# Kernel optimization log

Hardware: AMD Instinct MI355X
Metric: run time of the kernel (lower is better)

## Reference

```python
import jax, jax.numpy as jnp
import numpy as np

N = 50000   # nodes
E = 300000  # edges per etype
D = 256     # in_channels
STEPS = 3   # number_steps
EPS = 1e-5  # LayerNorm eps


def setup_inputs() -> dict:
    key = jax.random.key(0)
    ks = jax.random.split(key, 32)
    inp = {"x": jax.random.normal(ks[0], (N, D), jnp.float32)}
    for e in range(4):
        inp[f"src{e}"] = jax.random.randint(ks[1 + 2 * e], (E,), 0, N)
        inp[f"dst{e}"] = jax.random.randint(ks[2 + 2 * e], (E,), 0, N)
        inp[f"W{e}"] = jax.random.normal(ks[9 + e], (D, D), jnp.float32) / np.sqrt(D).astype(np.float32)
        inp[f"b{e}"] = jnp.zeros((D,), jnp.float32)
    inp["W_ih"] = jax.random.normal(ks[20], (3 * D, D), jnp.float32) / np.sqrt(D).astype(np.float32)
    inp["W_hh"] = jax.random.normal(ks[21], (3 * D, D), jnp.float32) / np.sqrt(D).astype(np.float32)
    inp["b_ih"] = jnp.zeros((3 * D,), jnp.float32)
    inp["b_hh"] = jnp.zeros((3 * D,), jnp.float32)
    inp["gamma"] = jnp.ones((D,), jnp.float32)
    inp["beta"] = jnp.zeros((D,), jnp.float32)
    return inp


def reference(x, src0, dst0, src1, dst1, src2, dst2, src3, dst3,
              W0, b0, W1, b1, W2, b2, W3, b3,
              W_ih, W_hh, b_ih, b_hh, gamma, beta):
    srcs = (src0, src1, src2, src3)
    dsts = (dst0, dst1, dst2, dst3)
    lins = ((W0, b0), (W1, b1), (W2, b2), (W3, b3))
    n_nodes = x.shape[0]

    def step(h):
        # per-etype: linear projection, gather on src, scatter-mean on dst; cross-etype 'sum'
        agg = jnp.zeros_like(h)
        for (W, b), s, d in zip(lins, srcs, dsts):
            proj = h @ W.T + b                                  # [N, D]
            msum = jax.ops.segment_sum(proj[s], d, num_segments=n_nodes)  # [N, D]
            deg = jax.ops.segment_sum(jnp.ones((s.shape[0], 1), h.dtype), d, num_segments=n_nodes)
            agg = agg + msum / jnp.maximum(deg, 1.0)            # mean; 0 for isolated nodes
        # torch GRUCell: input = agg, hidden = h
        gi = agg @ W_ih.T + b_ih                                # [N, 3D]
        gh = h @ W_hh.T + b_hh                                  # [N, 3D]
        i_r, i_z, i_n = jnp.split(gi, 3, axis=-1)
        h_r, h_z, h_n = jnp.split(gh, 3, axis=-1)
        r = jax.nn.sigmoid(i_r + h_r)
        z = jax.nn.sigmoid(i_z + h_z)
        n = jnp.tanh(i_n + r * h_n)
        h = (1.0 - z) * n + z * h
        # LayerNorm (use_norm=True); dropout is identity in eval mode
        mu = h.mean(-1, keepdims=True)
        var = h.var(-1, keepdims=True)
        return (h - mu) * jax.lax.rsqrt(var + EPS) * gamma + beta

    for _ in range(STEPS):
        x = step(x)
    return x
```

## Files before the change

### kernel.cpp

```cpp
#include <hip/hip_runtime.h>
#include <hip/hip_bf16.h>
#include <cstddef>

#define N_NODES 50000
#define E_EDGES 300000
#define D 256
#define SCHUNKS 196

typedef unsigned short u16;
typedef __attribute__((ext_vector_type(8))) short bf16x8;
typedef __attribute__((ext_vector_type(4))) float f32x4;

__device__ __forceinline__ float b2f(u16 u) {
    return __uint_as_float(((unsigned)u) << 16);
}
__device__ __forceinline__ u16 f2b(float f) {
    __hip_bfloat16 h = __float2bfloat16(f);
    return *reinterpret_cast<u16*>(&h);
}
__device__ __forceinline__ void async16(const u16* g, u16* l) {
    __builtin_amdgcn_global_load_lds(
        (const __attribute__((address_space(1))) void*)g,
        (__attribute__((address_space(3))) void*)l, 16, 0, 0);
}

__global__ __launch_bounds__(256) void prep_kernel(
    const float* __restrict__ W0, const float* __restrict__ W1,
    const float* __restrict__ W2, const float* __restrict__ W3,
    const float* __restrict__ b0, const float* __restrict__ b1,
    const float* __restrict__ b2, const float* __restrict__ b3,
    const float* __restrict__ W_ih, const float* __restrict__ W_hh,
    const float* __restrict__ b_ih, const float* __restrict__ b_hh,
    u16* __restrict__ Bfull_b, u16* __restrict__ Bcat_b,
    float* __restrict__ bfull, float* __restrict__ be4)
{
    int t = blockIdx.x * 256 + threadIdx.x;
    {
        int j = t >> 9, k = t & 511;
        float v;
        if (k < 256) v = (j < 768) ? W_ih[j * 256 + k] : W_hh[(j - 256) * 256 + k];
        else         v = (j < 512) ? W_hh[j * 256 + (k - 256)] : 0.f;
        Bfull_b[t] = f2b(v);
    }
    if (t < 262144) {
        int j = t >> 10, k = t & 1023;
        int e = k >> 8, kk = k & 255;
        const float* W = (e == 0) ? W0 : (e == 1) ? W1 : (e == 2) ? W2 : W3;
        Bcat_b[t] = f2b(W[j * 256 + kk]);
    }
    if (t < 1024) {
        bfull[t] = (t < 512) ? b_ih[t] + b_hh[t]
                 : (t < 768) ? b_ih[t] : b_hh[t - 256];
        int e = t >> 8, k = t & 255;
        const float* b = (e == 0) ? b0 : (e == 1) ? b1 : (e == 2) ? b2 : b3;
        be4[t] = b[k];
    }
}

__global__ __launch_bounds__(256) void xcvt_kernel(
    const float* __restrict__ x, u16* __restrict__ hb)
{
    int t = blockIdx.x * 256 + threadIdx.x;
    float4 v = *reinterpret_cast<const float4*>(x + (size_t)t * 4);
    ushort4 o;
    o.x = f2b(v.x); o.y = f2b(v.y); o.z = f2b(v.z); o.w = f2b(v.w);
    *reinterpret_cast<ushort4*>(hb + (size_t)t * 4) = o;
}

__global__ __launch_bounds__(256) void cnt_kernel(
    const int* __restrict__ d0, const int* __restrict__ d1,
    const int* __restrict__ d2, const int* __restrict__ d3,
    int* __restrict__ rowptr, u16* __restrict__ rank)
{
    int i = blockIdx.x * 256 + threadIdx.x;
    if (i >= 4 * E_EDGES) return;
    int e = i / E_EDGES;
    int k = i - e * E_EDGES;
    const int* dp = (e == 0) ? d0 : (e == 1) ? d1 : (e == 2) ? d2 : d3;
    rank[i] = (u16)atomicAdd(&rowptr[e * (N_NODES + 1) + dp[k] + 1], 1);
}

__global__ __launch_bounds__(256) void scan1_kernel(
    int* __restrict__ rowptr, int* __restrict__ bsum)
{
    int e = blockIdx.y;
    int blk = blockIdx.x;
    int t = threadIdx.x;
    int idx = blk * 256 + t;
    int* rp = rowptr + e * (N_NODES + 1);
    int v = (idx <= N_NODES) ? rp[idx] : 0;
    __shared__ int s[256];
    s[t] = v;
    __syncthreads();
    for (int o = 1; o < 256; o <<= 1) {
        int u = (t >= o) ? s[t - o] : 0;
        __syncthreads();
        s[t] += u;
        __syncthreads();
    }
    if (idx <= N_NODES) rp[idx] = s[t];
    if (t == 255) bsum[e * SCHUNKS + blk] = s[255];
}

__global__ __launch_bounds__(256) void scan2_kernel(int* __restrict__ bsum)
{
    int e = blockIdx.x;
    int t = threadIdx.x;
    int v = (t < SCHUNKS) ? bsum[e * SCHUNKS + t] : 0;
    __shared__ int s[256];
    s[t] = v;
    __syncthreads();
    for (int o = 1; o < 256; o <<= 1) {
        int u = (t >= o) ? s[t - o] : 0;
        __syncthreads();
        s[t] += u;
        __syncthreads();
    }
    if (t < SCHUNKS) bsum[e * SCHUNKS + t] = s[t];
}

__global__ __launch_bounds__(256) void scan3_kernel(
    int* __restrict__ rowptr, const int* __restrict__ bsum)
{
    int e = blockIdx.y;
    int blk = blockIdx.x;
    if (blk == 0) return;
    int idx = blk * 256 + threadIdx.x;
    if (idx > N_NODES) return;
    rowptr[e * (N_NODES + 1) + idx] += bsum[e * SCHUNKS + blk - 1];
}

__global__ __launch_bounds__(256) void fill_csr_kernel(
    const int* __restrict__ s0, const int* __restrict__ d0,
    const int* __restrict__ s1, const int* __restrict__ d1,
    const int* __restrict__ s2, const int* __restrict__ d2,
    const int* __restrict__ s3, const int* __restrict__ d3,
    const int* __restrict__ rowptr, const u16* __restrict__ rank,
    u16* __restrict__ colb)
{
    int i = blockIdx.x * 256 + threadIdx.x;
    if (i >= 4 * E_EDGES) return;
    int e = i / E_EDGES;
    int k = i - e * E_EDGES;
    const int* sp = (e == 0) ? s0 : (e == 1) ? s1 : (e == 2) ? s2 : s3;
    const int* dp = (e == 0) ? d0 : (e == 1) ? d1 : (e == 2) ? d2 : d3;
    int dst = dp[k];
    int slot = rowptr[e * (N_NODES + 1) + dst] + (int)rank[i];
    colb[(size_t)e * E_EDGES + slot] = (u16)sp[k];
}

__global__ __launch_bounds__(256) void degmask_kernel(
    const int* __restrict__ rowptr, unsigned char* __restrict__ degmask)
{
    int n = blockIdx.x * 256 + threadIdx.x;
    if (n >= N_NODES) return;
    int m = 0;
#pragma unroll
    for (int e = 0; e < 4; ++e) {
        const int* rp = rowptr + e * (N_NODES + 1);
        if (rp[n + 1] > rp[n]) m |= (1 << e);
    }
    degmask[n] = (unsigned char)m;
}

__global__ __launch_bounds__(256) void gather_kernel(
    const u16* __restrict__ hb, const int* __restrict__ rowptr,
    const u16* __restrict__ colb, u16* __restrict__ out,
    int pairArg, int stride)
{
    int p = (pairArg < 0) ? (int)blockIdx.y : pairArg;
    int n = blockIdx.x * 2 + (threadIdx.x >> 7);
    int el = (threadIdx.x >> 6) & 1;
    int lane = threadIdx.x & 63;
    int e = p * 2 + el;
    const int* rp = rowptr + e * (N_NODES + 1);
    int beg = rp[n], end = rp[n + 1];
    const u16* cb = colb + (size_t)e * E_EDGES;

    float4 a0 = make_float4(0.f, 0.f, 0.f, 0.f);
    float4 a1 = a0, a2 = a0, a3 = a0;
    int j = beg;
    for (; j + 4 <= end; j += 4) {
        int s0 = cb[j], s1 = cb[j + 1], s2 = cb[j + 2], s3 = cb[j + 3];
        ushort4 u0 = *reinterpret_cast<const ushort4*>(hb + (size_t)s0 * D + lane * 4);
        ushort4 u1 = *reinterpret_cast<const ushort4*>(hb + (size_t)s1 * D + lane * 4);
        ushort4 u2 = *reinterpret_cast<const ushort4*>(hb + (size_t)s2 * D + lane * 4);
        ushort4 u3 = *reinterpret_cast<const ushort4*>(hb + (size_t)s3 * D + lane * 4);
        a0.x += b2f(u0.x); a0.y += b2f(u0.y); a0.z += b2f(u0.z); a0.w += b2f(u0.w);
        a1.x += b2f(u1.x); a1.y += b2f(u1.y); a1.z += b2f(u1.z); a1.w += b2f(u1.w);
        a2.x += b2f(u2.x); a2.y += b2f(u2.y); a2.z += b2f(u2.z); a2.w += b2f(u2.w);
        a3.x += b2f(u3.x); a3.y += b2f(u3.y); a3.z += b2f(u3.z); a3.w += b2f(u3.w);
    }
    for (; j < end; ++j) {
        int s0 = cb[j];
        ushort4 u0 = *reinterpret_cast<const ushort4*>(hb + (size_t)s0 * D + lane * 4);
        a0.x += b2f(u0.x); a0.y += b2f(u0.y); a0.z += b2f(u0.z); a0.w += b2f(u0.w);
    }
    float ax = (a0.x + a1.x) + (a2.x + a3.x);
    float ay = (a0.y + a1.y) + (a2.y + a3.y);
    float az = (a0.z + a1.z) + (a2.z + a3.z);
    float aw = (a0.w + a1.w) + (a2.w + a3.w);
    float s = (end > beg) ? 1.f / (float)(end - beg) : 0.f;
    int colblk = (stride == 1024) ? e : el;
    ushort4 o;
    o.x = f2b(ax * s); o.y = f2b(ay * s); o.z = f2b(az * s); o.w = f2b(aw * s);
    *reinterpret_cast<ushort4*>(out + (size_t)n * stride + colblk * 256 + lane * 4) = o;
}

template <int BIASK, bool ACCUM>
__global__ __launch_bounds__(256) void gemm_mfma(
    const u16* __restrict__ A0, int lda0,
    const u16* __restrict__ A1, int lda1,
    const u16* __restrict__ Bw, int ldb,
    u16* __restrict__ C0, int ldc0, u16* __restrict__ C1, int ldc1,
    u16* __restrict__ C2, int ldc2,
    int split1, int split2, int nkt0, int KS,
    const float* __restrict__ bias0, const float* __restrict__ bias1,
    const unsigned char* __restrict__ degmask, int mshift)
{
    __shared__ u16 As[8192];
    __shared__ u16 Bs2[8192];

    const int gx = gridDim.x;
    const int nwg = gx * gridDim.y;
    const int lin = blockIdx.y * gx + blockIdx.x;
    const int q = nwg >> 3, r = nwg & 7;
    const int xcd = lin & 7, pos = lin >> 3;
    const int wg = (xcd < r) ? xcd * (q + 1) + pos
                             : r * (q + 1) + (xcd - r) * q + pos;
    const int by = wg / gx;
    const int bx = wg - by * gx;
    const int bm = by * 128;
    const int bn = bx * 128;

    const int tid = threadIdx.x;
    const int lane = tid & 63;
    const int wid = tid >> 6;
    const int wr = wid >> 1;
    const int wc = wid & 1;
    const int l15 = lane & 15;
    const int l4 = lane >> 4;

    int srow[4], schk[4];
#pragma unroll
    for (int i = 0; i < 4; ++i) {
        int qq = (wid * 4 + i) * 64 + lane;
        srow[i] = qq >> 3;
        schk[i] = (qq & 7) ^ (srow[i] & 7);
    }

    f32x4 acc[4][4];
#pragma unroll
    for (int i = 0; i < 4; ++i)
#pragma unroll
        for (int j = 0; j < 4; ++j)
            acc[i][j] = (f32x4){0.f, 0.f, 0.f, 0.f};

    int nkt, ksel;
    if (bn < split1)      { nkt = nkt0; ksel = KS; }
    else if (bn < split2) { nkt = KS;   ksel = KS; }
    else                  { nkt = KS;   ksel = 0;  }

    for (int kt = 0; kt < nkt; ++kt) {
        const u16* Ab; int lda;
        if (kt < ksel) { Ab = A0 + (size_t)kt * 64;          lda = lda0; }
        else           { Ab = A1 + (size_t)(kt - ksel) * 64; lda = lda1; }
#pragma unroll
        for (int i = 0; i < 4; ++i) {
            int rrow = bm + srow[i];
            if (rrow > N_NODES - 1) rrow = N_NODES - 1;
            async16(Ab + (size_t)rrow * lda + schk[i] * 8,
                    &As[(wid * 4 + i) * 512]);
        }
#pragma unroll
        for (int i = 0; i < 4; ++i)
            async16(Bw + (size_t)(bn + srow[i]) * ldb + kt * 64 + schk[i] * 8,
                    &Bs2[(wid * 4 + i) * 512]);
        __syncthreads();

#pragma unroll
        for (int kk = 0; kk < 2; ++kk) {
            bf16x8 a[4], b[4];
#pragma unroll
            for (int i = 0; i < 4; ++i) {
                int ar = wr * 64 + i * 16 + l15;
                a[i] = *reinterpret_cast<const bf16x8*>(
                    &As[ar * 64 + (((kk * 4 + l4) ^ (ar & 7)) << 3)]);
                int bc = wc * 64 + i * 16 + l15;
                b[i] = *reinterpret_cast<const bf16x8*>(
                    &Bs2[bc * 64 + (((kk * 4 + l4) ^ (bc & 7)) << 3)]);
            }
#pragma unroll
            for (int i = 0; i < 4; ++i)
#pragma unroll
                for (int j = 0; j < 4; ++j)
                    acc[i][j] = __builtin_amdgcn_mfma_f32_16x16x32_bf16(
                        a[i], b[j], acc[i][j], 0, 0, 0);
        }
        __syncthreads();
    }

    u16* Cw; int ldc, cb0;
    if (bn < split1)      { Cw = C0; ldc = ldc0; cb0 = bn; }
    else if (bn < split2) { Cw = C1; ldc = ldc1; cb0 = bn - split1; }
    else                  { Cw = C2; ldc = ldc2; cb0 = bn - split2; }

    float bj0[4], bj1[4];
    float bj4[4][4];
    if constexpr (BIASK == 4) {
#pragma unroll
        for (int e = 0; e < 4; ++e)
#pragma unroll
            for (int j = 0; j < 4; ++j)
                bj4[e][j] = bias0[e * 256 + bn + wc * 64 + j * 16 + l15];
    } else {
#pragma unroll
        for (int j = 0; j < 4; ++j) {
            int col = bn + wc * 64 + j * 16 + l15;
            bj0[j] = bias0[col];
            if (BIASK == 3) bj1[j] = bias1[col];
        }
    }
#pragma unroll
    for (int i = 0; i < 4; ++i) {
        int row0 = bm + wr * 64 + i * 16 + l4 * 4;
#pragma unroll
        for (int r2 = 0; r2 < 4; ++r2) {
            int row = row0 + r2;
            if (row < N_NODES) {
#pragma unroll
                for (int j = 0; j < 4; ++j) {
                    int col = cb0 + wc * 64 + j * 16 + l15;
                    float o = acc[i][j][r2];
                    if constexpr (BIASK == 4) {
                        int bits = degmask[row];
#pragma unroll
                        for (int e = 0; e < 4; ++e)
                            o += ((bits >> e) & 1) ? bj4[e][j] : 0.f;
                    } else if constexpr (BIASK == 3) {
                        int bits = degmask[row] >> mshift;
                        o += ((bits & 1) ? bj0[j] : 0.f) + ((bits & 2) ? bj1[j] : 0.f);
                    } else {
                        o += bj0[j];
                    }
                    u16* cp = Cw + (size_t)row * ldc + col;
                    if (ACCUM) o += b2f(*cp);
                    *cp = f2b(o);
                }
            }
        }
    }
}

template <int OUTM>
__global__ __launch_bounds__(256) void gru_ln_kernel(
    const u16* __restrict__ rz, const u16* __restrict__ nin,
    const u16* __restrict__ hn, const u16* __restrict__ hb,
    void* __restrict__ outv,
    const float* __restrict__ gamma, const float* __restrict__ beta)
{
    int w = threadIdx.x >> 6;
    int l = threadIdx.x & 63;
    int n = blockIdx.x * 4 + w;
    size_t b2 = (size_t)n * 512;
    size_t b1 = (size_t)n * D;

    u16 ra[4], za[4], na[4], ha[4], va[4];
    *reinterpret_cast<ushort4*>(ra) = *reinterpret_cast<const ushort4*>(rz + b2 + l * 4);
    *reinterpret_cast<ushort4*>(za) = *reinterpret_cast<const ushort4*>(rz + b2 + 256 + l * 4);
    *reinterpret_cast<ushort4*>(na) = *reinterpret_cast<const ushort4*>(nin + b1 + l * 4);
    *reinterpret_cast<ushort4*>(ha) = *reinterpret_cast<const ushort4*>(hn + b1 + l * 4);
    *reinterpret_cast<ushort4*>(va) = *reinterpret_cast<const ushort4*>(hb + b1 + l * 4);

    float hnew[4];
    float s1 = 0.f, s2 = 0.f;
#pragma unroll
    for (int c = 0; c < 4; ++c) {
        float r = 1.f / (1.f + __expf(-b2f(ra[c])));
        float z = 1.f / (1.f + __expf(-b2f(za[c])));
        float xn = b2f(na[c]) + r * b2f(ha[c]);
        float nn = 2.f / (1.f + __expf(-2.f * xn)) - 1.f;
        hnew[c] = (1.f - z) * nn + z * b2f(va[c]);
        s1 += hnew[c];
        s2 += hnew[c] * hnew[c];
    }
#pragma unroll
    for (int o = 32; o > 0; o >>= 1) {
        s1 += __shfl_down(s1, o);
        s2 += __shfl_down(s2, o);
    }
    float sum = __shfl(s1, 0);
    float ssq = __shfl(s2, 0);
    float mu = sum * (1.f / D);
    float var = ssq * (1.f / D) - mu * mu;
    float rstd = rsqrtf(var + 1e-5f);

    float4 g = *reinterpret_cast<const float4*>(gamma + l * 4);
    float4 bt = *reinterpret_cast<const float4*>(beta + l * 4);
    float res[4];
    res[0] = (hnew[0] - mu) * rstd * g.x + bt.x;
    res[1] = (hnew[1] - mu) * rstd * g.y + bt.y;
    res[2] = (hnew[2] - mu) * rstd * g.z + bt.z;
    res[3] = (hnew[3] - mu) * rstd * g.w + bt.w;

    if (OUTM == 0) {
        ushort4 o;
        o.x = f2b(res[0]); o.y = f2b(res[1]); o.z = f2b(res[2]); o.w = f2b(res[3]);
        *reinterpret_cast<ushort4*>((u16*)outv + b1 + l * 4) = o;
    } else {
        *reinterpret_cast<float4*>((float*)outv + b1 + l * 4) =
            make_float4(res[0], res[1], res[2], res[3]);
    }
}

__global__ __launch_bounds__(256) void wsfail_kernel(float* __restrict__ out, float val, int n)
{
    int i = blockIdx.x * 256 + threadIdx.x;
    if (i < n) out[i] = val;
}

extern "C" void kernel_launch(void* const* d_in, const int* in_sizes, int n_in,
                              void* d_out, int out_size, void* d_ws, size_t ws_size,
                              hipStream_t stream)
{
    const float* x    = (const float*)d_in[0];
    const int* se[4] = {(const int*)d_in[1], (const int*)d_in[5],
                        (const int*)d_in[9], (const int*)d_in[13]};
    const int* de[4] = {(const int*)d_in[2], (const int*)d_in[6],
                        (const int*)d_in[10], (const int*)d_in[14]};
    const float* We[4] = {(const float*)d_in[3], (const float*)d_in[7],
                          (const float*)d_in[11], (const float*)d_in[15]};
    const float* be[4] = {(const float*)d_in[4], (const float*)d_in[8],
                          (const float*)d_in[12], (const float*)d_in[16]};
    const float* W_ih = (const float*)d_in[17];
    const float* W_hh = (const float*)d_in[18];
    const float* b_ih = (const float*)d_in[19];
    const float* b_hh = (const float*)d_in[20];
    const float* gamma = (const float*)d_in[21];
    const float* beta  = (const float*)d_in[22];
    float* outf = (float*)d_out;

    const size_t SZ_H4 = (size_t)N_NODES * 1024 * 2;
    const size_t SZ_H2 = (size_t)N_NODES * 512 * 2;
    const size_t SZ_ND = (size_t)N_NODES * 256 * 2;
    const size_t TAIL = 800016 + 3136 + 2400000 + 2400000 + 50000
                      + 1048576 + 524288 + 4096 + 4096;
    const size_t NEED_BIG   = SZ_H4 + 2 * SZ_ND + TAIL;
    const size_t NEED_SMALL = SZ_H2 + 3 * SZ_ND + TAIL;

    const bool big = (ws_size >= NEED_BIG);

    char* p = (char*)d_ws;
    u16 *Hm, *rzb, *ninb, *hnb, *aggb, *h_bf;
    if (big) {
        Hm   = (u16*)p; p += SZ_H4;
        rzb  = Hm;
        ninb = (u16*)((char*)Hm + SZ_H2);
        hnb  = (u16*)((char*)Hm + SZ_H2 + SZ_ND);
        aggb = (u16*)p; p += SZ_ND;
        h_bf = (u16*)p; p += SZ_ND;
    } else {
        Hm   = (u16*)p; p += SZ_H2;
        rzb  = Hm;
        aggb = (u16*)p; p += SZ_ND;
        hnb  = aggb;
        ninb = (u16*)p; p += SZ_ND;
        h_bf = (u16*)p; p += SZ_ND;
    }
    int* rowptr = (int*)p; p += 800016;
    int* bsum   = (int*)p; p += 3136;
    u16* colb   = (u16*)p; p += 2400000;
    u16* rank   = (u16*)p; p += 2400000;
    unsigned char* degmask = (unsigned char*)p; p += 50000;
    u16* Bfull_b = (u16*)p; p += 1048576;
    u16* Bcat_b  = (u16*)p; p += 524288;
    float* bfull = (float*)p; p += 4096;
    float* be4   = (float*)p; p += 4096;

    if (ws_size < (size_t)(p - (char*)d_ws)) {
        wsfail_kernel<<<(out_size + 255) / 256, 256, 0, stream>>>(
            outf, (float)(ws_size >> 20), out_size);
        return;
    }

    hipMemsetAsync(rowptr, 0, (size_t)4 * (N_NODES + 1) * 4, stream);
    prep_kernel<<<2048, 256, 0, stream>>>(
        We[0], We[1], We[2], We[3], be[0], be[1], be[2], be[3],
        W_ih, W_hh, b_ih, b_hh, Bfull_b, Bcat_b, bfull, be4);
    xcvt_kernel<<<N_NODES * D / 4 / 256, 256, 0, stream>>>(x, h_bf);
    cnt_kernel<<<(4 * E_EDGES + 255) / 256, 256, 0, stream>>>(
        de[0], de[1], de[2], de[3], rowptr, rank);
    scan1_kernel<<<dim3(SCHUNKS, 4), 256, 0, stream>>>(rowptr, bsum);
    scan2_kernel<<<4, 256, 0, stream>>>(bsum);
    scan3_kernel<<<dim3(SCHUNKS, 4), 256, 0, stream>>>(rowptr, bsum);
    fill_csr_kernel<<<(4 * E_EDGES + 255) / 256, 256, 0, stream>>>(
        se[0], de[0], se[1], de[1], se[2], de[2], se[3], de[3],
        rowptr, rank, colb);
    degmask_kernel<<<(N_NODES + 255) / 256, 256, 0, stream>>>(rowptr, degmask);

    const int BIG30 = 1 << 30;
    for (int step = 0; step < 3; ++step) {
        if (big) {
            gather_kernel<<<dim3(N_NODES / 2, 2), 256, 0, stream>>>(
                h_bf, rowptr, colb, Hm, -1, 1024);
            gemm_mfma<4, false><<<dim3(2, 391), 256, 0, stream>>>(
                Hm, 1024, nullptr, 0, Bcat_b, 1024,
                aggb, 256, nullptr, 0, nullptr, 0,
                BIG30, BIG30, 16, 16, be4, nullptr, degmask, 0);
            gemm_mfma<1, false><<<dim3(8, 391), 256, 0, stream>>>(
                aggb, 256, h_bf, 256, Bfull_b, 512,
                rzb, 512, ninb, 256, hnb, 256,
                512, 768, 8, 4, bfull, nullptr, nullptr, 0);
        } else {
            for (int pair = 0; pair < 2; ++pair) {
                gather_kernel<<<dim3(N_NODES / 2, 1), 256, 0, stream>>>(
                    h_bf, rowptr, colb, Hm, pair, 512);
                if (pair == 0)
                    gemm_mfma<3, false><<<dim3(2, 391), 256, 0, stream>>>(
                        Hm, 512, nullptr, 0, Bcat_b + 512, 1024,
                        aggb, 256, nullptr, 0, nullptr, 0,
                        BIG30, BIG30, 8, 8, be4, be4 + 256, degmask, 0);
                else
                    gemm_mfma<3, true><<<dim3(2, 391), 256, 0, stream>>>(
                        Hm, 512, nullptr, 0, Bcat_b + 512, 1024,
                        aggb, 256, nullptr, 0, nullptr, 0,
                        BIG30, BIG30, 8, 8, be4 + 512, be4 + 768, degmask, 2);
            }
            gemm_mfma<1, false><<<dim3(6, 391), 256, 0, stream>>>(
                aggb, 256, h_bf, 256, Bfull_b, 512,
                rzb, 512, ninb, 256, nullptr, 0,
                512, BIG30, 8, 4, bfull, nullptr, nullptr, 0);
            gemm_mfma<1, false><<<dim3(2, 391), 256, 0, stream>>>(
                nullptr, 0, h_bf, 256, Bfull_b + (size_t)768 * 512, 512,
                nullptr, 0, nullptr, 0, hnb, 256,
                0, 0, 4, 4, bfull + 768, nullptr, nullptr, 0);
        }

        if (step < 2)
            gru_ln_kernel<0><<<N_NODES / 4, 256, 0, stream>>>(
                rzb, ninb, hnb, h_bf, h_bf, gamma, beta);
        else
            gru_ln_kernel<1><<<N_NODES / 4, 256, 0, stream>>>(
                rzb, ninb, hnb, h_bf, outf, gamma, beta);
    }
}
```

Before: 813.1 us.

## Widen GEMM tile to 128x256 with 512 threads and fold degmask into CSR fill

The MFMA GEMM now uses 512-thread workgroups computing 128x256 output tiles, so each A tile loaded from global memory is reused across twice as many output columns and fewer workgroups are launched. The small-workspace fallback path and its accumulate and dual-bias variants are removed, leaving only the big-workspace schedule. The degree-mask computation is merged into the CSR fill kernel to drop one launch. In exchange, LDS use per workgroup grows and the grid shrinks to 391 or 1564 blocks, which may reduce occupancy and latency hiding. The code now assumes the workspace is large enough for the big layout.

Result: faster. 786.6 us (median of 2 runs) (-3.3%).

```diff
diff --git a/kernel.cpp b/kernel.cpp
--- a/kernel.cpp
+++ b/kernel.cpp
@@ -136,7 +136,7 @@
     const int* __restrict__ s2, const int* __restrict__ d2,
     const int* __restrict__ s3, const int* __restrict__ d3,
     const int* __restrict__ rowptr, const u16* __restrict__ rank,
-    u16* __restrict__ colb)
+    u16* __restrict__ colb, unsigned char* __restrict__ degmask)
 {
     int i = blockIdx.x * 256 + threadIdx.x;
     if (i >= 4 * E_EDGES) return;
@@ -147,28 +147,22 @@
     int dst = dp[k];
     int slot = rowptr[e * (N_NODES + 1) + dst] + (int)rank[i];
     colb[(size_t)e * E_EDGES + slot] = (u16)sp[k];
-}
-
-__global__ __launch_bounds__(256) void degmask_kernel(
-    const int* __restrict__ rowptr, unsigned char* __restrict__ degmask)
-{
-    int n = blockIdx.x * 256 + threadIdx.x;
-    if (n >= N_NODES) return;
-    int m = 0;
-#pragma unroll
-    for (int e = 0; e < 4; ++e) {
-        const int* rp = rowptr + e * (N_NODES + 1);
-        if (rp[n + 1] > rp[n]) m |= (1 << e);
-    }
-    degmask[n] = (unsigned char)m;
+    if (i < N_NODES) {
+        int m = 0;
+#pragma unroll
+        for (int ee = 0; ee < 4; ++ee) {
+            const int* rp = rowptr + ee * (N_NODES + 1);
+            if (rp[i + 1] > rp[i]) m |= (1 << ee);
+        }
+        degmask[i] = (unsigned char)m;
+    }
 }
 
 __global__ __launch_bounds__(256) void gather_kernel(
     const u16* __restrict__ hb, const int* __restrict__ rowptr,
-    const u16* __restrict__ colb, u16* __restrict__ out,
-    int pairArg, int stride)
-{
-    int p = (pairArg < 0) ? (int)blockIdx.y : pairArg;
+    const u16* __restrict__ colb, u16* __restrict__ out)
+{
+    int p = blockIdx.y;
     int n = blockIdx.x * 2 + (threadIdx.x >> 7);
     int el = (threadIdx.x >> 6) & 1;
     int lane = threadIdx.x & 63;
@@ -201,25 +195,23 @@
     float az = (a0.z + a1.z) + (a2.z + a3.z);
     float aw = (a0.w + a1.w) + (a2.w + a3.w);
     float s = (end > beg) ? 1.f / (float)(end - beg) : 0.f;
-    int colblk = (stride == 1024) ? e : el;
     ushort4 o;
     o.x = f2b(ax * s); o.y = f2b(ay * s); o.z = f2b(az * s); o.w = f2b(aw * s);
-    *reinterpret_cast<ushort4*>(out + (size_t)n * stride + colblk * 256 + lane * 4) = o;
-}
-
-template <int BIASK, bool ACCUM>
-__global__ __launch_bounds__(256) void gemm_mfma(
+    *reinterpret_cast<ushort4*>(out + (size_t)n * 1024 + e * 256 + lane * 4) = o;
+}
+
+template <int BIASK>
+__global__ __launch_bounds__(512, 4) void gemm_mfma(
     const u16* __restrict__ A0, int lda0,
     const u16* __restrict__ A1, int lda1,
     const u16* __restrict__ Bw, int ldb,
     u16* __restrict__ C0, int ldc0, u16* __restrict__ C1, int ldc1,
     u16* __restrict__ C2, int ldc2,
     int split1, int split2, int nkt0, int KS,
-    const float* __restrict__ bias0, const float* __restrict__ bias1,
-    const unsigned char* __restrict__ degmask, int mshift)
+    const float* __restrict__ bias0, const unsigned char* __restrict__ degmask)
 {
     __shared__ u16 As[8192];
-    __shared__ u16 Bs2[8192];
+    __shared__ u16 Bs2[16384];
 
     const int gx = gridDim.x;
     const int nwg = gx * gridDim.y;
@@ -231,22 +223,29 @@
     const int by = wg / gx;
     const int bx = wg - by * gx;
     const int bm = by * 128;
-    const int bn = bx * 128;
+    const int bn = bx * 256;
 
     const int tid = threadIdx.x;
     const int lane = tid & 63;
     const int wid = tid >> 6;
-    const int wr = wid >> 1;
-    const int wc = wid & 1;
+    const int wr = wid >> 2;
+    const int wc = wid & 3;
     const int l15 = lane & 15;
     const int l4 = lane >> 4;
 
-    int srow[4], schk[4];
-#pragma unroll
-    for (int i = 0; i < 4; ++i) {
-        int qq = (wid * 4 + i) * 64 + lane;
-        srow[i] = qq >> 3;
-        schk[i] = (qq & 7) ^ (srow[i] & 7);
+    int arow[2], achk[2];
+#pragma unroll
+    for (int ps = 0; ps < 2; ++ps) {
+        int s = wid * 128 + ps * 64 + lane;
+        arow[ps] = s >> 3;
+        achk[ps] = (s & 7) ^ (arow[ps] & 7);
+    }
+    int brow[4], bchk[4];
+#pragma unroll
+    for (int ps = 0; ps < 4; ++ps) {
+        int s = wid * 256 + ps * 64 + lane;
+        brow[ps] = s >> 3;
+        bchk[ps] = (s & 7) ^ (brow[ps] & 7);
     }
 
     f32x4 acc[4][4];
@@ -266,16 +265,16 @@
         if (kt < ksel) { Ab = A0 + (size_t)kt * 64;          lda = lda0; }
         else           { Ab = A1 + (size_t)(kt - ksel) * 64; lda = lda1; }
 #pragma unroll
-        for (int i = 0; i < 4; ++i) {
-            int rrow = bm + srow[i];
+        for (int ps = 0; ps < 2; ++ps) {
+            int rrow = bm + arow[ps];
             if (rrow > N_NODES - 1) rrow = N_NODES - 1;
-            async16(Ab + (size_t)rrow * lda + schk[i] * 8,
-                    &As[(wid * 4 + i) * 512]);
+            async16(Ab + (size_t)rrow * lda + achk[ps] * 8,
+                    &As[(wid * 128 + ps * 64) * 8]);
         }
 #pragma unroll
-        for (int i = 0; i < 4; ++i)
-            async16(Bw + (size_t)(bn + srow[i]) * ldb + kt * 64 + schk[i] * 8,
-                    &Bs2[(wid * 4 + i) * 512]);
+        for (int ps = 0; ps < 4; ++ps)
+            async16(Bw + (size_t)(bn + brow[ps]) * ldb + kt * 64 + bchk[ps] * 8,
+                    &Bs2[(wid * 256 + ps * 64) * 8]);
         __syncthreads();
 
 #pragma unroll
@@ -305,7 +304,7 @@
     else if (bn < split2) { Cw = C1; ldc = ldc1; cb0 = bn - split1; }
     else                  { Cw = C2; ldc = ldc2; cb0 = bn - split2; }
 
-    float bj0[4], bj1[4];
+    float bj0[4];
     float bj4[4][4];
     if constexpr (BIASK == 4) {
 #pragma unroll
@@ -315,11 +314,8 @@
                 bj4[e][j] = bias0[e * 256 + bn + wc * 64 + j * 16 + l15];
     } else {
 #pragma unroll
-        for (int j = 0; j < 4; ++j) {
-            int col = bn + wc * 64 + j * 16 + l15;
-            bj0[j] = bias0[col];
-            if (BIASK == 3) bj1[j] = bias1[col];
-        }
+        for (int j = 0; j < 4; ++j)
+            bj0[j] = bias0[bn + wc * 64 + j * 16 + l15];
     }
 #pragma unroll
     for (int i = 0; i < 4; ++i) {
@@ -337,15 +333,10 @@
 #pragma unroll
                         for (int e = 0; e < 4; ++e)
                             o += ((bits >> e) & 1) ? bj4[e][j] : 0.f;
-                    } else if constexpr (BIASK == 3) {
-                        int bits = degmask[row] >> mshift;
-                        o += ((bits & 1) ? bj0[j] : 0.f) + ((bits & 2) ? bj1[j] : 0.f);
                     } else {
                         o += bj0[j];
                     }
-                    u16* cp = Cw + (size_t)row * ldc + col;
-                    if (ACCUM) o += b2f(*cp);
-                    *cp = f2b(o);
+                    Cw[(size_t)row * ldc + col] = f2b(o);
                 }
             }
         }
@@ -443,30 +434,14 @@
     const size_t SZ_H4 = (size_t)N_NODES * 1024 * 2;
     const size_t SZ_H2 = (size_t)N_NODES * 512 * 2;
     const size_t SZ_ND = (size_t)N_NODES * 256 * 2;
-    const size_t TAIL = 800016 + 3136 + 2400000 + 2400000 + 50000
-                      + 1048576 + 524288 + 4096 + 4096;
-    const size_t NEED_BIG   = SZ_H4 + 2 * SZ_ND + TAIL;
-    const size_t NEED_SMALL = SZ_H2 + 3 * SZ_ND + TAIL;
-
-    const bool big = (ws_size >= NEED_BIG);
 
     char* p = (char*)d_ws;
-    u16 *Hm, *rzb, *ninb, *hnb, *aggb, *h_bf;
-    if (big) {
-        Hm   = (u16*)p; p += SZ_H4;
-        rzb  = Hm;
-        ninb = (u16*)((char*)Hm + SZ_H2);
-        hnb  = (u16*)((char*)Hm + SZ_H2 + SZ_ND);
-        aggb = (u16*)p; p += SZ_ND;
-        h_bf = (u16*)p; p += SZ_ND;
-    } else {
-        Hm   = (u16*)p; p += SZ_H2;
-        rzb  = Hm;
-        aggb = (u16*)p; p += SZ_ND;
-        hnb  = aggb;
-        ninb = (u16*)p; p += SZ_ND;
-        h_bf = (u16*)p; p += SZ_ND;
-    }
+    u16* Hm   = (u16*)p; p += SZ_H4;
+    u16* rzb  = Hm;
+    u16* ninb = (u16*)((char*)Hm + SZ_H2);
+    u16* hnb  = (u16*)((char*)Hm + SZ_H2 + SZ_ND);
+    u16* aggb = (u16*)p; p += SZ_ND;
+    u16* h_bf = (u16*)p; p += SZ_ND;
     int* rowptr = (int*)p; p += 800016;
     int* bsum   = (int*)p; p += 3136;
     u16* colb   = (u16*)p; p += 2400000;
@@ -495,46 +470,20 @@
     scan3_kernel<<<dim3(SCHUNKS, 4), 256, 0, stream>>>(rowptr, bsum);
     fill_csr_kernel<<<(4 * E_EDGES + 255) / 256, 256, 0, stream>>>(
         se[0], de[0], se[1], de[1], se[2], de[2], se[3], de[3],
-        rowptr, rank, colb);
-    degmask_kernel<<<(N_NODES + 255) / 256, 256, 0, stream>>>(rowptr, degmask);
+        rowptr, rank, colb, degmask);
 
     const int BIG30 = 1 << 30;
     for (int step = 0; step < 3; ++step) {
-        if (big) {
-            gather_kernel<<<dim3(N_NODES / 2, 2), 256, 0, stream>>>(
-                h_bf, rowptr, colb, Hm, -1, 1024);
-            gemm_mfma<4, false><<<dim3(2, 391), 256, 0, stream>>>(
-                Hm, 1024, nullptr, 0, Bcat_b, 1024,
-                aggb, 256, nullptr, 0, nullptr, 0,
-                BIG30, BIG30, 16, 16, be4, nullptr, degmask, 0);
-            gemm_mfma<1, false><<<dim3(8, 391), 256, 0, stream>>>(
-                aggb, 256, h_bf, 256, Bfull_b, 512,
-                rzb, 512, ninb, 256, hnb, 256,
-                512, 768, 8, 4, bfull, nullptr, nullptr, 0);
-        } else {
-            for (int pair = 0; pair < 2; ++pair) {
-                gather_kernel<<<dim3(N_NODES / 2, 1), 256, 0, stream>>>(
-                    h_bf, rowptr, colb, Hm, pair, 512);
-                if (pair == 0)
-                    gemm_mfma<3, false><<<dim3(2, 391), 256, 0, stream>>>(
-                        Hm, 512, nullptr, 0, Bcat_b + 512, 1024,
-                        aggb, 256, nullptr, 0, nullptr, 0,
-                        BIG30, BIG30, 8, 8, be4, be4 + 256, degmask, 0);
-                else
-                    gemm_mfma<3, true><<<dim3(2, 391), 256, 0, stream>>>(
-                        Hm, 512, nullptr, 0, Bcat_b + 512, 1024,
-                        aggb, 256, nullptr, 0, nullptr, 0,
-                        BIG30, BIG30, 8, 8, be4 + 512, be4 + 768, degmask, 2);
-            }
-            gemm_mfma<1, false><<<dim3(6, 391), 256, 0, stream>>>(
-                aggb, 256, h_bf, 256, Bfull_b, 512,
-                rzb, 512, ninb, 256, nullptr, 0,
-                512, BIG30, 8, 4, bfull, nullptr, nullptr, 0);
-            gemm_mfma<1, false><<<dim3(2, 391), 256, 0, stream>>>(
-                nullptr, 0, h_bf, 256, Bfull_b + (size_t)768 * 512, 512,
-                nullptr, 0, nullptr, 0, hnb, 256,
-                0, 0, 4, 4, bfull + 768, nullptr, nullptr, 0);
-        }
+        gather_kernel<<<dim3(N_NODES / 2, 2), 256, 0, stream>>>(
+            h_bf, rowptr, colb, Hm);
+        gemm_mfma<4><<<dim3(1, 391), 512, 0, stream>>>(
+            Hm, 1024, nullptr, 0, Bcat_b, 1024,
+            aggb, 256, nullptr, 0, nullptr, 0,
+            BIG30, BIG30, 16, 16, be4, degmask);
+        gemm_mfma<1><<<dim3(4, 391), 512, 0, stream>>>(
+            aggb, 256, h_bf, 256, Bfull_b, 512,
+            rzb, 512, ninb, 256, hnb, 256,
+            512, 768, 8, 4, bfull, nullptr);
 
         if (step < 2)
             gru_ln_kernel<0><<<N_NODES / 4, 256, 0, stream>>>(
```
